# Kernel tuning notes

Hardware: AMD Instinct MI355X
Metric: run time of the kernel (lower is better)

## Reference

```python
import jax, jax.numpy as jnp
import numpy as np
from jax import lax

G, K, C_IN, C_FEAT, H, W, B = 8, 6, 512, 256, 64, 64, 1


def apply_offset(offset):
    # offset: [N, 2, H, W] pixel-space offsets -> sampling grid [N, H, W, 2] in [-1, 1]
    # channel 0 displaces x (width), channel 1 displaces y (height), matching the
    # reversed-meshgrid logic of the original torch apply_offset.
    n, _, h, w = offset.shape
    jj = jnp.arange(w, dtype=offset.dtype)[None, None, :]
    ii = jnp.arange(h, dtype=offset.dtype)[None, :, None]
    gx = (jj + offset[:, 0]) / ((w - 1.0) / 2.0) - 1.0
    gy = (ii + offset[:, 1]) / ((h - 1.0) / 2.0) - 1.0
    return jnp.stack([gx, gy], axis=-1)


def grid_sample_border(img, grid):
    # img: [N, C, H, W], grid: [N, H, W, 2] in [-1, 1]
    # Bilinear, padding_mode='border', align_corners=False (torch grid_sample default).
    n, c, h, w = img.shape
    x = jnp.clip((grid[..., 0] + 1.0) * w * 0.5 - 0.5, 0.0, w - 1.0)
    y = jnp.clip((grid[..., 1] + 1.0) * h * 0.5 - 0.5, 0.0, h - 1.0)
    x0 = jnp.floor(x)
    y0 = jnp.floor(y)
    wx = (x - x0)[:, None]  # [N,1,H,W]
    wy = (y - y0)[:, None]
    x0i = x0.astype(jnp.int32)
    y0i = y0.astype(jnp.int32)
    x1i = jnp.minimum(x0i + 1, w - 1)
    y1i = jnp.minimum(y0i + 1, h - 1)

    def gather(im, yi, xi):  # im [C,H,W]; yi, xi [H,W]
        return im[:, yi, xi]

    g = jax.vmap(gather)
    v00 = g(img, y0i, x0i)
    v01 = g(img, y0i, x1i)
    v10 = g(img, y1i, x0i)
    v11 = g(img, y1i, x1i)
    return (1.0 - wy) * ((1.0 - wx) * v00 + wx * v01) + wy * ((1.0 - wx) * v10 + wx * v11)


def setup_inputs() -> dict:
    key = jax.random.key(0)
    ks = jax.random.split(key, 11)
    s = 0.02
    return {
        "gar_feat": jax.random.normal(ks[0], (B, C_FEAT, H, W), jnp.float32),
        "cond_feat": jax.random.normal(ks[1], (B, C_FEAT, H, W), jnp.float32),
        "mask": jax.random.uniform(ks[2], (B, G, C_FEAT), dtype=jnp.float32),
        "W1": jax.random.normal(ks[3], (G, 128, C_IN, 3, 3), jnp.float32) * s,
        "b1": jax.random.normal(ks[4], (G, 128), jnp.float32) * s,
        "W2": jax.random.normal(ks[5], (G, 64, 128, 3, 3), jnp.float32) * s,
        "b2": jax.random.normal(ks[6], (G, 64), jnp.float32) * s,
        "W3": jax.random.normal(ks[7], (G, 32, 64, 3, 3), jnp.float32) * s,
        "b3": jax.random.normal(ks[8], (G, 32), jnp.float32) * s,
        "W4": jax.random.normal(ks[9], (G, 3 * K, 32, 3, 3), jnp.float32) * s,
        "b4": jax.random.normal(ks[10], (G, 3 * K), jnp.float32) * s,
    }


def reference(gar_feat, cond_feat, mask, W1, b1, W2, b2, W3, b3, W4, b4):
    b, c, h, w = gar_feat.shape
    g = W1.shape[0]
    k = W4.shape[1] // 3
    inp = jnp.concatenate([gar_feat, cond_feat], axis=1)  # [B, 2C, H, W]

    def conv(x, wgt, bias):
        return lax.conv_general_dilated(
            x, wgt, (1, 1), 'SAME', dimension_numbers=('NCHW', 'OIHW', 'NCHW')
        ) + bias[None, :, None, None]

    def lrelu(x):
        return jnp.where(x >= 0, x, 0.1 * x)

    def group_net(w1, bb1, w2, bb2, w3, bb3, w4, bb4):
        hid = lrelu(conv(inp, w1, bb1))
        hid = lrelu(conv(hid, w2, bb2))
        hid = lrelu(conv(hid, w3, bb3))
        return conv(hid, w4, bb4)  # [B, 3k, H, W]

    oa = jax.vmap(group_net)(W1, b1, W2, b2, W3, b3, W4, b4)  # [G, B, 3k, H, W]
    attn = jax.nn.softmax(oa[:, :, 2 * k:], axis=0)           # softmax across groups: [G,B,k,H,W]
    off = oa[:, :, :2 * k].reshape(g, b * k, 2, h, w)
    grid = jax.vmap(apply_offset)(off)                        # [G, B*k, H, W, 2]

    rep = jnp.repeat(gar_feat, k, axis=0)                     # [B*k, C, H, W]

    def warp_group(grid_g, attn_g, mask_g):
        samp = grid_sample_border(rep, grid_g).reshape(b, k, c, h, w)
        wfeat = jnp.sum(samp * attn_g[:, :, None], axis=1)    # [B, C, H, W]
        return wfeat * mask_g[:, :, None, None]

    warped = jax.vmap(warp_group)(grid, attn, jnp.transpose(mask, (1, 0, 2)))
    return jnp.sum(warped, axis=0)  # [B, C, H, W]
```

## Files before the change

### kernel.cpp

```cpp
#include <hip/hip_runtime.h>
#include <hip/hip_bf16.h>

typedef __hip_bfloat16 bf16;
typedef unsigned short ushort8v __attribute__((ext_vector_type(8)));
typedef short  s16x4  __attribute__((ext_vector_type(4)));
typedef short  bf16x8 __attribute__((ext_vector_type(8)));
typedef float  f32x4  __attribute__((ext_vector_type(4)));

#define HW 4096
#define IMG_W 64

__device__ __forceinline__ float bfbits2f(unsigned short u) {
    return __uint_as_float(((unsigned int)u) << 16);
}
__device__ __forceinline__ short f2bs(float f) {
    bf16 h = __float2bfloat16(f);
    return *reinterpret_cast<short*>(&h);
}

__device__ __forceinline__ void gl_lds16(const void* g, void* s) {
    __builtin_amdgcn_global_load_lds(
        (const __attribute__((address_space(1))) unsigned int*)g,
        (__attribute__((address_space(3))) unsigned int*)s, 16, 0, 0);
}

__device__ void pack_input_dev(const float* __restrict__ gar,
                               const float* __restrict__ cond,
                               short* __restrict__ outp, int bx2, float* tile)
{
    int bx = bx2 & 127;
    int by = bx2 >> 7;
    int tx = threadIdx.x & 31;
    int ty = threadIdx.x >> 5;
#pragma unroll
    for (int i = 0; i < 4; ++i) {
        int c = by * 32 + ty + i * 8;
        const float* src = (c < 256) ? (gar + (size_t)c * HW)
                                     : (cond + (size_t)(c - 256) * HW);
        tile[(ty + i * 8) * 33 + tx] = src[bx * 32 + tx];
    }
    __syncthreads();
#pragma unroll
    for (int i = 0; i < 4; ++i) {
        int p = bx * 32 + ty + i * 8;
        outp[((size_t)by * 4096 + p) * 32 + tx] = f2bs(tile[tx * 33 + ty + i * 8]);
    }
}

template<int CIN, int CREAL, int BN, int NT, bool COAL>
__device__ void pack_w_dev(const float* __restrict__ wgt, char* __restrict__ wp,
                           int bx, short* sT)
{
    constexpr int NCC  = CIN / 32;
    constexpr int BLKB = 9 * 4 * BN * 16;

    const int t  = threadIdx.x;
    const int cc = bx % NCC;
    const int nt = (bx / NCC) % NT;
    const int g  = bx / (NT * NCC);

    for (int i = t; i < BLKB / 8; i += 256)
        reinterpret_cast<s16x4*>(sT)[i] = s16x4{0, 0, 0, 0};
    __syncthreads();

    int ocmax = CREAL - nt * BN; if (ocmax > BN) ocmax = BN;
    const size_t base = ((size_t)(g * CREAL + nt * BN) * CIN + cc * 32) * 9;
    for (int i = t; i < ocmax * 288; i += 256) {
        int oc = i / 288;
        int r  = i % 288;
        int ic = r / 9, tap = r % 9;
        size_t idx;
        if (COAL) idx = (size_t)(((tap * BN + oc) * 4 + (ic >> 3)) * 8 + (ic & 7));
        else      idx = (size_t)(((tap * 4 + (ic >> 3)) * BN + oc) * 8 + (ic & 7));
        sT[idx] = f2bs(wgt[base + (size_t)oc * CIN * 9 + r]);
    }
    __syncthreads();

    const s16x4* src = reinterpret_cast<const s16x4*>(sT);
    s16x4* dst = reinterpret_cast<s16x4*>(wp + (size_t)bx * BLKB);
    for (int i = t; i < BLKB / 8; i += 256)
        dst[i] = src[i];
}

__global__ __launch_bounds__(256)
void pack_all(const float* __restrict__ gar, const float* __restrict__ cond,
              const float* __restrict__ W1, const float* __restrict__ W2,
              const float* __restrict__ W3, const float* __restrict__ W4,
              short* inp_t, char* W1p, char* W2p, char* W3p, char* W4p)
{
    __shared__ __align__(16) short sbuf[9 * 4 * 64 * 8];
    int bx = blockIdx.x;
    if (bx < 256)      pack_w_dev<512, 128, 64, 2, true >(W1, W1p, bx,       sbuf);
    else if (bx < 288) pack_w_dev<128,  64, 64, 1, false>(W2, W2p, bx - 256, sbuf);
    else if (bx < 304) pack_w_dev< 64,  32, 32, 1, false>(W3, W3p, bx - 288, sbuf);
    else if (bx < 312) pack_w_dev< 32,  18, 32, 1, false>(W4, W4p, bx - 304, sbuf);
    else pack_input_dev(gar, cond, inp_t, bx - 312, (float*)sbuf);
}

template<int ICP, int CREAL, int BN, int ROWS, int OF, int NT, int NW, int PIPE,
         bool PIXMAJ_OUT, bool LEAKY, bool OUT_F32>
__global__ __launch_bounds__(NW * 64, 2)
void conv_mfma(const short* __restrict__ inp, const char* __restrict__ wp,
               const float* __restrict__ bias, void* __restrict__ outv)
{
    constexpr int NCC  = ICP / 32;
    constexpr int HALO = ROWS + 2;
    constexpr int NPT  = 4096 / (ROWS * 64);
    constexpr int BLKB = 9 * 4 * BN * 16;
    constexpr int RNDS = BLKB / 1024;
    constexpr int NBUF = (PIPE && NCC > 1) ? 2 : 1;
    constexpr int SMAX = (HALO + NW - 1) / NW;

    __shared__ __align__(16) short sA[HALO][4][68][8];
    __shared__ __align__(16) char  sBraw[NBUF][BLKB];

    const int b  = blockIdx.x;
    const int g  = b & 7;
    const int r_ = b >> 3;
    const int pt = r_ % NPT;
    const int nt = r_ / NPT;
    const int r0 = pt * ROWS;

    const int t    = threadIdx.x;
    const int wave = t >> 6, lane = t & 63;
    const int l15  = lane & 15, quad = lane >> 4;

    int row_l, ocw;
    if (NW == 8) {
        if (ROWS == 4) { row_l = wave >> 1; ocw = (wave & 1) * (BN / 2); }
        else           { row_l = wave >> 2; ocw = (wave & 3) * (BN / 4); }
    } else {
        row_l = (ROWS == 4) ? wave : (wave & 1);
        ocw   = (ROWS == 4) ? 0 : (wave >> 1) * (BN / 2);
    }

    const size_t gpix = (ICP == 512) ? 0 : ((size_t)g * 4096);
    const char*  wb   = wp + (size_t)((g * NT + nt) * NCC) * BLKB;

    const int acol = t & 63;
    const int r2   = t >> 6;

    bf16x8 pre[SMAX][4];

    auto stageA_load = [&](int cc) {
#pragma unroll
        for (int s = 0; s < SMAX; ++s) {
            int j = r2 + s * NW;
            if (j < HALO) {
                int gy = r0 - 1 + j;
                if (gy >= 0 && gy < 64) {
                    const short* sp = inp + ((gpix + gy * 64 + acol) * ICP + cc * 32);
#pragma unroll
                    for (int q = 0; q < 4; ++q)
                        pre[s][q] = *reinterpret_cast<const bf16x8*>(sp + q * 8);
                } else {
#pragma unroll
                    for (int q = 0; q < 4; ++q)
                        pre[s][q] = bf16x8{0, 0, 0, 0, 0, 0, 0, 0};
                }
            }
        }
    };
    auto stageA_write = [&]() {
#pragma unroll
        for (int s = 0; s < SMAX; ++s) {
            int j = r2 + s * NW;
            if (j < HALO) {
#pragma unroll
                for (int q = 0; q < 4; ++q)
                    *reinterpret_cast<bf16x8*>(&sA[j][q][acol + 1][0]) = pre[s][q];
            }
        }
    };
    auto stageB = [&](int cc) {
        const char* wsrc = wb + (size_t)cc * BLKB;
        char* sbb = (char*)sBraw[(NBUF == 2) ? (cc & 1) : 0];
        for (int r = wave; r < RNDS; r += NW)
            gl_lds16(wsrc + r * 1024 + lane * 16, sbb + r * 1024);
    };

    f32x4 acc[OF][4];
#pragma unroll
    for (int o = 0; o < OF; ++o)
#pragma unroll
        for (int p = 0; p < 4; ++p)
#pragma unroll
            for (int r = 0; r < 4; ++r) acc[o][p][r] = 0.f;

    if (t < HALO * 8) {
        int row = t >> 3, q = (t >> 1) & 3, cp = (t & 1) ? 65 : 0;
        *reinterpret_cast<bf16x8*>(&sA[row][q][cp][0]) =
            bf16x8{0, 0, 0, 0, 0, 0, 0, 0};
    }

    stageB(0);
    stageA_load(0);
    stageA_write();

    for (int cc = 0; cc < NCC; ++cc) {
        __syncthreads();
        if (cc + 1 < NCC) {
            if (PIPE) stageB(cc + 1);
            stageA_load(cc + 1);
        }
        const bf16x8* sBv = reinterpret_cast<const bf16x8*>(
            sBraw[(NBUF == 2) ? (cc & 1) : 0]);

#pragma unroll
        for (int dy = 0; dy < 3; ++dy) {
#pragma unroll
            for (int dx = 0; dx < 3; ++dx) {
                bf16x8 pF[4];
#pragma unroll
                for (int p = 0; p < 4; ++p)
                    pF[p] = *reinterpret_cast<const bf16x8*>(
                        &sA[row_l + dy][quad][p * 16 + l15 + dx][0]);
                bf16x8 wF[OF];
#pragma unroll
                for (int o = 0; o < OF; ++o)
                    wF[o] = sBv[((dy * 3 + dx) * 4 + quad) * BN + ocw + o * 16 + l15];
#pragma unroll
                for (int o = 0; o < OF; ++o)
#pragma unroll
                    for (int p = 0; p < 4; ++p)
                        acc[o][p] = __builtin_amdgcn_mfma_f32_16x16x32_bf16(
                            wF[o], pF[p], acc[o][p], 0, 0, 0);
            }
        }
        __syncthreads();
        if (cc + 1 < NCC) {
            if (!PIPE) stageB(cc + 1);
            stageA_write();
        }
    }

    const int prow = r0 + row_l;
#pragma unroll
    for (int o = 0; o < OF; ++o)
#pragma unroll
        for (int reg = 0; reg < 4; ++reg) {
            const int ocl = ocw + o * 16 + quad * 4 + reg;
            const int ocg = nt * BN + ocl;
            if (ocg < CREAL) {
                const float bv = bias[g * CREAL + ocg];
                if (PIXMAJ_OUT) {
                    short* outp = (short*)outv;
                    const size_t pixbase = ((size_t)g * 4096 + prow * 64);
#pragma unroll
                    for (int p = 0; p < 4; ++p) {
                        float v = acc[o][p][reg] + bv;
                        if (LEAKY) v = v >= 0.f ? v : 0.1f * v;
                        outp[(pixbase + p * 16 + l15) * (NT * BN) + ocg] = f2bs(v);
                    }
                } else if (OUT_F32) {
                    float* outp = (float*)outv;
                    const size_t base = ((size_t)(g * CREAL + ocg)) * HW + prow * IMG_W;
#pragma unroll
                    for (int p = 0; p < 4; ++p) {
                        float v = acc[o][p][reg] + bv;
                        if (LEAKY) v = v >= 0.f ? v : 0.1f * v;
                        outp[base + p * 16 + l15] = v;
                    }
                } else {
                    short* outp = (short*)outv;
                    const size_t base = ((size_t)(g * CREAL + ocg)) * HW + prow * IMG_W;
#pragma unroll
                    for (int p = 0; p < 4; ++p) {
                        float v = acc[o][p][reg] + bv;
                        if (LEAKY) v = v >= 0.f ? v : 0.1f * v;
                        outp[base + p * 16 + l15] = f2bs(v);
                    }
                }
            }
        }
}

__global__ __launch_bounds__(256, 2)
void conv1_direct(const short* __restrict__ inp, const char* __restrict__ wp,
                  const float* __restrict__ bias, short* __restrict__ outp)
{
    __shared__ __align__(16) short sA[2][4][66][4][8];

    const int b  = blockIdx.x;
    const int g  = b & 7;
    const int r_ = b >> 3;
    const int pt = r_ & 31;
    const int nt = r_ >> 5;
    const int r0 = pt * 2;

    const int t    = threadIdx.x;
    const int wave = t >> 6, lane = t & 63;
    const int l15  = lane & 15, quad = lane >> 4;

    const int row_l = wave & 1;
    const int ocw   = (wave >> 1) * 32;

    const short* wb    = (const short*)wp + (size_t)(g * 2 + nt) * 16 * 18432;
    const short* wlane = wb + ((size_t)(ocw + l15) * 4 + quad) * 8;

    auto stageDMA = [&](int cc, int buf) {
        int gy = r0 - 1 + wave;
        if (gy >= 0 && gy < 64) {
            const short* src = inp + ((size_t)cc * 4096 + (size_t)gy * 64) * 32
                                   + (size_t)lane * 8;
#pragma unroll
            for (int c4 = 0; c4 < 4; ++c4)
                gl_lds16(src + c4 * 512, &sA[buf][wave][1 + c4 * 16][0][0]);
        }
    };

    bf16x8 wA[9][2], wB[9][2];
    auto loadW_into = [&](int cc, bf16x8 (&w)[9][2]) {
        const short* ws = wlane + (size_t)cc * 18432;
#pragma unroll
        for (int tap = 0; tap < 9; ++tap)
#pragma unroll
            for (int o = 0; o < 2; ++o)
                w[tap][o] = *reinterpret_cast<const bf16x8*>(
                    ws + tap * 2048 + o * 512);
    };

    f32x4 acc[2][4];
#pragma unroll
    for (int o = 0; o < 2; ++o)
#pragma unroll
        for (int p = 0; p < 4; ++p)
#pragma unroll
            for (int r = 0; r < 4; ++r) acc[o][p][r] = 0.f;

    loadW_into(0, wA);
    stageDMA(0, 0);
    if (t < 64) {
        int buf = t >> 5, row = (t >> 3) & 3, q = (t >> 1) & 3;
        int col = (t & 1) ? 65 : 0;
        *reinterpret_cast<bf16x8*>(&sA[buf][row][col][q][0]) =
            bf16x8{0, 0, 0, 0, 0, 0, 0, 0};
    }
    if (r0 == 0 || r0 == 62) {
        int zr = (r0 == 0) ? 0 : 3;
        for (int i = t; i < 2 * 66 * 4; i += 256) {
            int buf = i / 264, rem = i % 264;
            *reinterpret_cast<bf16x8*>(&sA[buf][zr][rem >> 2][rem & 3][0]) =
                bf16x8{0, 0, 0, 0, 0, 0, 0, 0};
        }
    }

    auto body = [&](int cc, int cur, bf16x8 (&wuse)[9][2], bf16x8 (&wld)[9][2]) {
        __syncthreads();
        if (cc + 1 < 16) {
            stageDMA(cc + 1, cur ^ 1);
            loadW_into(cc + 1, wld);
        }
#pragma unroll
        for (int dy = 0; dy < 3; ++dy)
#pragma unroll
            for (int dx = 0; dx < 3; ++dx) {
                bf16x8 pF[4];
#pragma unroll
                for (int p = 0; p < 4; ++p)
                    pF[p] = *reinterpret_cast<const bf16x8*>(
                        &sA[cur][row_l + dy][p * 16 + l15 + dx][quad][0]);
#pragma unroll
                for (int o = 0; o < 2; ++o)
#pragma unroll
                    for (int p = 0; p < 4; ++p)
                        acc[o][p] = __builtin_amdgcn_mfma_f32_16x16x32_bf16(
                            wuse[dy * 3 + dx][o], pF[p], acc[o][p], 0, 0, 0);
            }
    };

    for (int c2 = 0; c2 < 16; c2 += 2) {
        body(c2,     0, wA, wB);
        body(c2 + 1, 1, wB, wA);
    }

    const int prow = r0 + row_l;
    const size_t pixbase = (size_t)g * 4096 + (size_t)prow * 64;
#pragma unroll
    for (int o = 0; o < 2; ++o)
#pragma unroll
        for (int reg = 0; reg < 4; ++reg) {
            const int ocg = nt * 64 + ocw + o * 16 + quad * 4 + reg;
            const float bv = bias[g * 128 + ocg];
#pragma unroll
            for (int p = 0; p < 4; ++p) {
                float v = acc[o][p][reg] + bv;
                v = v >= 0.f ? v : 0.1f * v;
                outp[(pixbase + p * 16 + l15) * 128 + ocg] = f2bs(v);
            }
        }
}

__global__ __launch_bounds__(256)
void warp_combine_kernel(const float* __restrict__ oa,
                         const short* __restrict__ inp_t,
                         const float* __restrict__ mask,
                         float* __restrict__ out)
{
    __shared__ __align__(16) float4 sWts[8][6][8];
    __shared__ __align__(16) int4   sIdx[8][6][8];

    const int t = threadIdx.x;

    if (t < 48) {
        int lp = t / 6;
        int k  = t % 6;
        int p  = blockIdx.x * 8 + lp;
        int x  = p & 63, y = p >> 6;

        float l[8];
        float m = -1e30f;
#pragma unroll
        for (int g = 0; g < 8; ++g) {
            l[g] = oa[(size_t)(g * 18 + 12 + k) * HW + p];
            m = fmaxf(m, l[g]);
        }
        float s = 0.f;
#pragma unroll
        for (int g = 0; g < 8; ++g) { l[g] = __expf(l[g] - m); s += l[g]; }
        float inv = 1.f / s;

#pragma unroll
        for (int g = 0; g < 8; ++g) {
            float a  = l[g] * inv;
            float ox = oa[(size_t)(g * 18 + 2 * k)     * HW + p];
            float oy = oa[(size_t)(g * 18 + 2 * k + 1) * HW + p];
            float sx = fminf(fmaxf(((float)x + ox) * (64.f / 63.f) - 0.5f, 0.f), 63.f);
            float sy = fminf(fmaxf(((float)y + oy) * (64.f / 63.f) - 0.5f, 0.f), 63.f);
            float fx0 = floorf(sx), fy0 = floorf(sy);
            int   x0 = (int)fx0,    y0i = (int)fy0;
            float wx = sx - fx0,    wy = sy - fy0;
            int   x1 = min(x0 + 1, 63), y1 = min(y0i + 1, 63);
            sWts[lp][k][g] = make_float4(a * (1.f - wy) * (1.f - wx),
                                         a * (1.f - wy) * wx,
                                         a * wy * (1.f - wx),
                                         a * wy * wx);
            sIdx[lp][k][g] = make_int4(y0i * 64 + x0, y0i * 64 + x1,
                                       y1  * 64 + x0, y1  * 64 + x1);
        }
    }
    __syncthreads();

    const int lp = t >> 5;
    const int p  = blockIdx.x * 8 + lp;
    const int c0 = (t & 31) * 8;
    const short* ipc = inp_t + (size_t)(c0 >> 5) * (4096 * 32) + (c0 & 31);

    float acc[8];
#pragma unroll
    for (int j = 0; j < 8; ++j) acc[j] = 0.f;

    for (int g = 0; g < 8; ++g) {
        float4 m0 = *reinterpret_cast<const float4*>(mask + g * 256 + c0);
        float4 m1 = *reinterpret_cast<const float4*>(mask + g * 256 + c0 + 4);
        float mk[8] = {m0.x, m0.y, m0.z, m0.w, m1.x, m1.y, m1.z, m1.w};
#pragma unroll
        for (int k = 0; k < 6; ++k) {
            float4 w  = sWts[lp][k][g];
            int4   id = sIdx[lp][k][g];
            ushort8v v00 = *reinterpret_cast<const ushort8v*>(ipc + (size_t)id.x * 32);
            ushort8v v01 = *reinterpret_cast<const ushort8v*>(ipc + (size_t)id.y * 32);
            ushort8v v10 = *reinterpret_cast<const ushort8v*>(ipc + (size_t)id.z * 32);
            ushort8v v11 = *reinterpret_cast<const ushort8v*>(ipc + (size_t)id.w * 32);
#pragma unroll
            for (int j = 0; j < 8; ++j) {
                float sv = w.x * bfbits2f(v00[j]) + w.y * bfbits2f(v01[j])
                         + w.z * bfbits2f(v10[j]) + w.w * bfbits2f(v11[j]);
                acc[j] = fmaf(mk[j], sv, acc[j]);
            }
        }
    }
#pragma unroll
    for (int j = 0; j < 8; ++j)
        out[(size_t)(c0 + j) * HW + p] = acc[j];
}

extern "C" void kernel_launch(void* const* d_in, const int* in_sizes, int n_in,
                              void* d_out, int out_size, void* d_ws, size_t ws_size,
                              hipStream_t stream)
{
    (void)in_sizes; (void)n_in; (void)out_size; (void)ws_size;
    const float* gar  = (const float*)d_in[0];
    const float* cond = (const float*)d_in[1];
    const float* mask = (const float*)d_in[2];
    const float* W1   = (const float*)d_in[3];
    const float* b1   = (const float*)d_in[4];
    const float* W2   = (const float*)d_in[5];
    const float* b2   = (const float*)d_in[6];
    const float* W3   = (const float*)d_in[7];
    const float* b3   = (const float*)d_in[8];
    const float* W4   = (const float*)d_in[9];
    const float* b4   = (const float*)d_in[10];
    float* out = (float*)d_out;

    char* ws = (char*)d_ws;
    short* inp_t  = (short*)(ws);
    char*  W1p    = ws + (4u << 20);
    short* hid2_t = (short*)(ws + (4u << 20));
    short* hid3_t = (short*)(ws + (8u << 20));
    float* oa     = (float*)(ws + (10u << 20) + (512u << 10));
    char*  W2p    = ws + (14u << 20);
    char*  W3p    = ws + (15u << 20) + (512u << 10);
    char*  W4p    = ws + (16u << 20);
    short* hid1_t = (short*)(ws + (17u << 20));

    pack_all<<<2360, 256, 0, stream>>>(gar, cond, W1, W2, W3, W4,
                                       inp_t, W1p, W2p, W3p, W4p);

    conv1_direct<<<512, 256, 0, stream>>>(inp_t, W1p, b1, hid1_t);
    conv_mfma<128, 64, 64, 2, 1, 1, 8, 1, true, true, false>
        <<<256, 512, 0, stream>>>(hid1_t, W2p, b2, hid2_t);
    conv_mfma<64, 32, 32, 2, 1, 1, 4, 1, true, true, false>
        <<<256, 256, 0, stream>>>(hid2_t, W3p, b3, hid3_t);
    conv_mfma<32, 18, 32, 2, 1, 1, 4, 1, false, false, true>
        <<<256, 256, 0, stream>>>(hid3_t, W4p, b4, oa);

    warp_combine_kernel<<<512, 256, 0, stream>>>(oa, inp_t, mask, out);
}
```

Before: 204.6 us.

## Split conv1 input-channel reduction across two blocks with fp32 partials and finalize kernel

Adds a split-K version of the first grouped conv that divides the 16 input-channel chunks into two halves, doubling the grid to 1024 blocks. Each block writes fp32 partial sums, and a separate finalize kernel adds the two partials plus bias, applies leaky ReLU and converts to bf16. The aim is more parallelism and occupancy on the largest conv stage. The cost is an extra kernel launch and about 32 MB of fp32 partial traffic written and read back. The path only runs when the workspace is at least 60 MB, otherwise the original kernel is used.

```diff
diff --git a/kernel.cpp b/kernel.cpp
--- a/kernel.cpp
+++ b/kernel.cpp
@@ -389,6 +389,140 @@
                 outp[(pixbase + p * 16 + l15) * 128 + ocg] = f2bs(v);
             }
         }
+}
+
+__global__ __launch_bounds__(256, 4)
+void conv1_ks(const short* __restrict__ inp, const char* __restrict__ wp,
+              float* __restrict__ part0, float* __restrict__ part1)
+{
+    __shared__ __align__(16) short sA[2][4][66][4][8];
+
+    const int b  = blockIdx.x;
+    const int g  = b & 7;
+    const int r_ = b >> 3;
+    const int pt = r_ & 31;
+    const int nt = (r_ >> 5) & 1;
+    const int ks = r_ >> 6;
+    const int r0 = pt * 2;
+    const int cc0 = ks * 8;
+
+    const int t    = threadIdx.x;
+    const int wave = t >> 6, lane = t & 63;
+    const int l15  = lane & 15, quad = lane >> 4;
+
+    const int row_l = wave & 1;
+    const int ocw   = (wave >> 1) * 32;
+
+    const short* wb    = (const short*)wp + (size_t)(g * 2 + nt) * 16 * 18432;
+    const short* wlane = wb + ((size_t)(ocw + l15) * 4 + quad) * 8;
+
+    auto stageDMA = [&](int cc, int buf) {
+        int gy = r0 - 1 + wave;
+        if (gy >= 0 && gy < 64) {
+            const short* src = inp + ((size_t)cc * 4096 + (size_t)gy * 64) * 32
+                                   + (size_t)lane * 8;
+#pragma unroll
+            for (int c4 = 0; c4 < 4; ++c4)
+                gl_lds16(src + c4 * 512, &sA[buf][wave][1 + c4 * 16][0][0]);
+        }
+    };
+
+    f32x4 acc[2][4];
+#pragma unroll
+    for (int o = 0; o < 2; ++o)
+#pragma unroll
+        for (int p = 0; p < 4; ++p)
+#pragma unroll
+            for (int r = 0; r < 4; ++r) acc[o][p][r] = 0.f;
+
+    stageDMA(cc0, 0);
+    if (t < 64) {
+        int buf = t >> 5, row = (t >> 3) & 3, q = (t >> 1) & 3;
+        int col = (t & 1) ? 65 : 0;
+        *reinterpret_cast<bf16x8*>(&sA[buf][row][col][q][0]) =
+            bf16x8{0, 0, 0, 0, 0, 0, 0, 0};
+    }
+    if (r0 == 0 || r0 == 62) {
+        int zr = (r0 == 0) ? 0 : 3;
+        for (int i = t; i < 2 * 66 * 4; i += 256) {
+            int buf = i / 264, rem = i % 264;
+            *reinterpret_cast<bf16x8*>(&sA[buf][zr][rem >> 2][rem & 3][0]) =
+                bf16x8{0, 0, 0, 0, 0, 0, 0, 0};
+        }
+    }
+
+    auto body = [&](int i, int cur) {
+        const int cc = cc0 + i;
+        __syncthreads();
+        if (i + 1 < 8) stageDMA(cc + 1, cur ^ 1);
+        const short* wcc = wlane + (size_t)cc * 18432;
+#pragma unroll
+        for (int dy = 0; dy < 3; ++dy)
+#pragma unroll
+            for (int dx = 0; dx < 3; ++dx) {
+                bf16x8 pF[4];
+#pragma unroll
+                for (int p = 0; p < 4; ++p)
+                    pF[p] = *reinterpret_cast<const bf16x8*>(
+                        &sA[cur][row_l + dy][p * 16 + l15 + dx][quad][0]);
+                bf16x8 w0 = *reinterpret_cast<const bf16x8*>(
+                    wcc + (dy * 3 + dx) * 2048);
+                bf16x8 w1 = *reinterpret_cast<const bf16x8*>(
+                    wcc + (dy * 3 + dx) * 2048 + 512);
+#pragma unroll
+                for (int p = 0; p < 4; ++p)
+                    acc[0][p] = __builtin_amdgcn_mfma_f32_16x16x32_bf16(
+                        w0, pF[p], acc[0][p], 0, 0, 0);
+#pragma unroll
+                for (int p = 0; p < 4; ++p)
+                    acc[1][p] = __builtin_amdgcn_mfma_f32_16x16x32_bf16(
+                        w1, pF[p], acc[1][p], 0, 0, 0);
+            }
+    };
+
+    for (int i2 = 0; i2 < 8; i2 += 2) {
+        body(i2,     0);
+        body(i2 + 1, 1);
+    }
+
+    float* pp = ks ? part1 : part0;
+    const int prow = r0 + row_l;
+    const size_t pixbase = (size_t)g * 4096 + (size_t)prow * 64;
+#pragma unroll
+    for (int o = 0; o < 2; ++o)
+#pragma unroll
+        for (int reg = 0; reg < 4; ++reg) {
+            const int ocg = nt * 64 + ocw + o * 16 + quad * 4 + reg;
+#pragma unroll
+            for (int p = 0; p < 4; ++p)
+                pp[(pixbase + p * 16 + l15) * 128 + ocg] = acc[o][p][reg];
+        }
+}
+
+__global__ __launch_bounds__(256)
+void finalize_conv1(const float* __restrict__ p0, const float* __restrict__ p1,
+                    const float* __restrict__ bias, short* __restrict__ outp)
+{
+    const size_t i8 = ((size_t)blockIdx.x * 256 + threadIdx.x) * 8;
+    const int oc0 = (int)(i8 & 127);
+    const int g   = (int)(i8 >> 19);
+    float4 a0 = *reinterpret_cast<const float4*>(p0 + i8);
+    float4 a1 = *reinterpret_cast<const float4*>(p0 + i8 + 4);
+    float4 b0 = *reinterpret_cast<const float4*>(p1 + i8);
+    float4 b1 = *reinterpret_cast<const float4*>(p1 + i8 + 4);
+    float4 c0 = *reinterpret_cast<const float4*>(bias + g * 128 + oc0);
+    float4 c1 = *reinterpret_cast<const float4*>(bias + g * 128 + oc0 + 4);
+    float v[8] = {a0.x + b0.x + c0.x, a0.y + b0.y + c0.y,
+                  a0.z + b0.z + c0.z, a0.w + b0.w + c0.w,
+                  a1.x + b1.x + c1.x, a1.y + b1.y + c1.y,
+                  a1.z + b1.z + c1.z, a1.w + b1.w + c1.w};
+    ushort8v r;
+#pragma unroll
+    for (int j = 0; j < 8; ++j) {
+        float x = v[j] >= 0.f ? v[j] : 0.1f * v[j];
+        r[j] = (unsigned short)f2bs(x);
+    }
+    *reinterpret_cast<ushort8v*>(outp + i8) = r;
 }
 
 __global__ __launch_bounds__(256)
@@ -479,7 +613,7 @@
                               void* d_out, int out_size, void* d_ws, size_t ws_size,
                               hipStream_t stream)
 {
-    (void)in_sizes; (void)n_in; (void)out_size; (void)ws_size;
+    (void)in_sizes; (void)n_in; (void)out_size;
     const float* gar  = (const float*)d_in[0];
     const float* cond = (const float*)d_in[1];
     const float* mask = (const float*)d_in[2];
@@ -503,11 +637,18 @@
     char*  W3p    = ws + (15u << 20) + (512u << 10);
     char*  W4p    = ws + (16u << 20);
     short* hid1_t = (short*)(ws + (17u << 20));
+    float* part0  = (float*)(ws + (28u << 20));
+    float* part1  = (float*)(ws + (44u << 20));
 
     pack_all<<<2360, 256, 0, stream>>>(gar, cond, W1, W2, W3, W4,
                                        inp_t, W1p, W2p, W3p, W4p);
 
-    conv1_direct<<<512, 256, 0, stream>>>(inp_t, W1p, b1, hid1_t);
+    if (ws_size >= ((size_t)60 << 20)) {
+        conv1_ks<<<1024, 256, 0, stream>>>(inp_t, W1p, part0, part1);
+        finalize_conv1<<<2048, 256, 0, stream>>>(part0, part1, b1, hid1_t);
+    } else {
+        conv1_direct<<<512, 256, 0, stream>>>(inp_t, W1p, b1, hid1_t);
+    }
     conv_mfma<128, 64, 64, 2, 1, 1, 8, 1, true, true, false>
         <<<256, 512, 0, stream>>>(hid1_t, W2p, b2, hid2_t);
     conv_mfma<64, 32, 32, 2, 1, 1, 4, 1, true, true, false>
```

Result: no change. 206.3 us (+0.8%).

## Merge conv1 output-channel halves into one 512-thread block with per-tap prefetch

Applied to the files above, without the earlier changes.

The first conv is restructured so each block covers all 128 output channels with 8 waves, instead of two separate blocks each handling 64 channels. The two channel halves now share one LDS input tile, so each input tile is staged once instead of twice. The weight double-buffer of 9 taps held in registers is replaced by a per-tap register ping-pong: the next tap's weights and LDS fragments are loaded while the current tap's MFMAs run, with a sched_barrier to keep that order. This lowers register pressure and redundant input traffic, but halves the block count to 256 and exposes per-tap weight-load latency.

```diff
diff --git a/kernel.cpp b/kernel.cpp
--- a/kernel.cpp
+++ b/kernel.cpp
@@ -275,17 +275,15 @@
         }
 }
 
-__global__ __launch_bounds__(256, 2)
-void conv1_direct(const short* __restrict__ inp, const char* __restrict__ wp,
-                  const float* __restrict__ bias, short* __restrict__ outp)
+__global__ __launch_bounds__(512, 2)
+void conv1_p2(const short* __restrict__ inp, const char* __restrict__ wp,
+              const float* __restrict__ bias, short* __restrict__ outp)
 {
     __shared__ __align__(16) short sA[2][4][66][4][8];
 
     const int b  = blockIdx.x;
     const int g  = b & 7;
-    const int r_ = b >> 3;
-    const int pt = r_ & 31;
-    const int nt = r_ >> 5;
+    const int pt = b >> 3;
     const int r0 = pt * 2;
 
     const int t    = threadIdx.x;
@@ -293,42 +291,33 @@
     const int l15  = lane & 15, quad = lane >> 4;
 
     const int row_l = wave & 1;
-    const int ocw   = (wave >> 1) * 32;
-
-    const short* wb    = (const short*)wp + (size_t)(g * 2 + nt) * 16 * 18432;
-    const short* wlane = wb + ((size_t)(ocw + l15) * 4 + quad) * 8;
+    const int ocq   = wave >> 1;
+    const int ntw   = ocq >> 1;
+    const int ocw64 = (ocq & 1) * 32;
+
+    const short* wb    = (const short*)wp + (size_t)(g * 2 + ntw) * 16 * 18432;
+    const short* wlane = wb + ((size_t)(ocw64 + l15) * 4 + quad) * 8;
 
     auto stageDMA = [&](int cc, int buf) {
-        int gy = r0 - 1 + wave;
+        const int row = wave >> 1;
+        const int gy  = r0 - 1 + row;
         if (gy >= 0 && gy < 64) {
             const short* src = inp + ((size_t)cc * 4096 + (size_t)gy * 64) * 32
                                    + (size_t)lane * 8;
-#pragma unroll
-            for (int c4 = 0; c4 < 4; ++c4)
-                gl_lds16(src + c4 * 512, &sA[buf][wave][1 + c4 * 16][0][0]);
+            const int c4 = (wave & 1) * 2;
+            gl_lds16(src + c4 * 512,       &sA[buf][row][1 + c4 * 16][0][0]);
+            gl_lds16(src + (c4 + 1) * 512, &sA[buf][row][1 + (c4 + 1) * 16][0][0]);
         }
     };
 
-    bf16x8 wA[9][2], wB[9][2];
-    auto loadW_into = [&](int cc, bf16x8 (&w)[9][2]) {
-        const short* ws = wlane + (size_t)cc * 18432;
-#pragma unroll
-        for (int tap = 0; tap < 9; ++tap)
-#pragma unroll
-            for (int o = 0; o < 2; ++o)
-                w[tap][o] = *reinterpret_cast<const bf16x8*>(
-                    ws + tap * 2048 + o * 512);
-    };
-
     f32x4 acc[2][4];
 #pragma unroll
     for (int o = 0; o < 2; ++o)
 #pragma unroll
-        for (int p = 0; p < 4; ++p)
-#pragma unroll
-            for (int r = 0; r < 4; ++r) acc[o][p][r] = 0.f;
-
-    loadW_into(0, wA);
+        for (int f = 0; f < 4; ++f)
+#pragma unroll
+            for (int r = 0; r < 4; ++r) acc[o][f][r] = 0.f;
+
     stageDMA(0, 0);
     if (t < 64) {
         int buf = t >> 5, row = (t >> 3) & 3, q = (t >> 1) & 3;
@@ -338,40 +327,55 @@
     }
     if (r0 == 0 || r0 == 62) {
         int zr = (r0 == 0) ? 0 : 3;
-        for (int i = t; i < 2 * 66 * 4; i += 256) {
+        for (int i = t; i < 2 * 66 * 4; i += 512) {
             int buf = i / 264, rem = i % 264;
             *reinterpret_cast<bf16x8*>(&sA[buf][zr][rem >> 2][rem & 3][0]) =
                 bf16x8{0, 0, 0, 0, 0, 0, 0, 0};
         }
     }
 
-    auto body = [&](int cc, int cur, bf16x8 (&wuse)[9][2], bf16x8 (&wld)[9][2]) {
+    bf16x8 w[2][2];
+    bf16x8 pf[2][4];
+#pragma unroll
+    for (int o = 0; o < 2; ++o)
+        w[0][o] = *reinterpret_cast<const bf16x8*>(wlane + o * 512);
+
+    auto body = [&](int cc, int cur, int par) {
+        const short* wcc = wlane + (size_t)cc * 18432;
         __syncthreads();
-        if (cc + 1 < 16) {
-            stageDMA(cc + 1, cur ^ 1);
-            loadW_into(cc + 1, wld);
-        }
-#pragma unroll
-        for (int dy = 0; dy < 3; ++dy)
-#pragma unroll
-            for (int dx = 0; dx < 3; ++dx) {
-                bf16x8 pF[4];
-#pragma unroll
-                for (int p = 0; p < 4; ++p)
-                    pF[p] = *reinterpret_cast<const bf16x8*>(
-                        &sA[cur][row_l + dy][p * 16 + l15 + dx][quad][0]);
-#pragma unroll
-                for (int o = 0; o < 2; ++o)
-#pragma unroll
-                    for (int p = 0; p < 4; ++p)
-                        acc[o][p] = __builtin_amdgcn_mfma_f32_16x16x32_bf16(
-                            wuse[dy * 3 + dx][o], pF[p], acc[o][p], 0, 0, 0);
-            }
+        if (cc + 1 < 16) stageDMA(cc + 1, cur ^ 1);
+#pragma unroll
+        for (int f = 0; f < 4; ++f)
+            pf[0][f] = *reinterpret_cast<const bf16x8*>(
+                &sA[cur][row_l][f * 16 + l15][quad][0]);
+#pragma unroll
+        for (int tap = 0; tap < 9; ++tap) {
+            const int pb = tap & 1, pn = pb ^ 1;
+            const int cb = (tap + par) & 1, nb = cb ^ 1;
+            if (tap < 8) {
+                const int dy1 = (tap + 1) / 3, dx1 = (tap + 1) % 3;
+#pragma unroll
+                for (int f = 0; f < 4; ++f)
+                    pf[pn][f] = *reinterpret_cast<const bf16x8*>(
+                        &sA[cur][row_l + dy1][f * 16 + l15 + dx1][quad][0]);
+            }
+            const short* nsrc = wcc + (size_t)(tap + 1) * 2048;
+#pragma unroll
+            for (int o = 0; o < 2; ++o)
+                w[nb][o] = *reinterpret_cast<const bf16x8*>(nsrc + o * 512);
+            __builtin_amdgcn_sched_barrier(0);
+#pragma unroll
+            for (int o = 0; o < 2; ++o)
+#pragma unroll
+                for (int f = 0; f < 4; ++f)
+                    acc[o][f] = __builtin_amdgcn_mfma_f32_16x16x32_bf16(
+                        w[cb][o], pf[pb][f], acc[o][f], 0, 0, 0);
+        }
     };
 
     for (int c2 = 0; c2 < 16; c2 += 2) {
-        body(c2,     0, wA, wB);
-        body(c2 + 1, 1, wB, wA);
+        body(c2,     0, 0);
+        body(c2 + 1, 1, 1);
     }
 
     const int prow = r0 + row_l;
@@ -380,13 +384,13 @@
     for (int o = 0; o < 2; ++o)
 #pragma unroll
         for (int reg = 0; reg < 4; ++reg) {
-            const int ocg = nt * 64 + ocw + o * 16 + quad * 4 + reg;
+            const int ocg = ocq * 32 + o * 16 + quad * 4 + reg;
             const float bv = bias[g * 128 + ocg];
 #pragma unroll
-            for (int p = 0; p < 4; ++p) {
-                float v = acc[o][p][reg] + bv;
+            for (int f = 0; f < 4; ++f) {
+                float v = acc[o][f][reg] + bv;
                 v = v >= 0.f ? v : 0.1f * v;
-                outp[(pixbase + p * 16 + l15) * 128 + ocg] = f2bs(v);
+                outp[(pixbase + f * 16 + l15) * 128 + ocg] = f2bs(v);
             }
         }
 }
@@ -507,7 +511,7 @@
     pack_all<<<2360, 256, 0, stream>>>(gar, cond, W1, W2, W3, W4,
                                        inp_t, W1p, W2p, W3p, W4p);
 
-    conv1_direct<<<512, 256, 0, stream>>>(inp_t, W1p, b1, hid1_t);
+    conv1_p2<<<256, 512, 0, stream>>>(inp_t, W1p, b1, hid1_t);
     conv_mfma<128, 64, 64, 2, 1, 1, 8, 1, true, true, false>
         <<<256, 512, 0, stream>>>(hid1_t, W2p, b2, hid2_t);
     conv_mfma<64, 32, 32, 2, 1, 1, 4, 1, true, true, false>
```

New measurement: 199.8 us. 1.02x faster.
